# Kernel tuning notes

Measured on AMD Instinct MI355X. Metric: run time of the kernel, lower is better.

The kernel has to match this reference:

```python
import jax, jax.numpy as jnp
import numpy as np

EPS = 1e-6  # epsilon used to snap near-zero plane distances (Moller-style robustness)


def _interval(p, d):
    """Interval of the intersection line covered by a triangle.
    p: [..., 3] projections of the 3 vertices onto the intersection-line axis.
    d: [..., 3] signed distances of the 3 vertices to the other triangle's plane.
    Returns (tmin, tmax); invalid (non-straddling) -> (+inf, -inf).
    """
    nxt = jnp.array([1, 2, 0])
    di, dj = d, d[..., nxt]
    pi, pj = p, p[..., nxt]
    # edge crosses the plane iff endpoint distances have opposite signs
    # (or exactly one endpoint lies on the plane)
    valid = (di * dj <= 0) & ~((di == 0) & (dj == 0))
    denom = di - dj
    t = pi + (pj - pi) * di / jnp.where(denom == 0, 1.0, denom)
    tmin = jnp.min(jnp.where(valid, t, jnp.inf), axis=-1)
    tmax = jnp.max(jnp.where(valid, t, -jnp.inf), axis=-1)
    return tmin, tmax


def _pairwise_intersect(T):
    """Moller-style triangle-triangle intersection test for all N^2 pairs.
    T: [N, 3, 3] triangle soup. Returns bool [N, N].
    """
    N = T.shape[0]
    n = jnp.cross(T[:, 1] - T[:, 0], T[:, 2] - T[:, 0])   # [N,3] plane normals
    d = -jnp.sum(n * T[:, 0], axis=-1)                      # [N] plane offsets
    # signed distances: verts of triangle b to plane of triangle u (dv), and vice versa (du)
    dv = jnp.einsum('bvc,nc->bnv', T, n) + d[None, :, None]  # [N,N,3]
    du = jnp.einsum('nvc,bc->bnv', T, n) + d[:, None, None]  # [N,N,3]
    dv = jnp.where(jnp.abs(dv) < EPS, 0.0, dv)
    du = jnp.where(jnp.abs(du) < EPS, 0.0, du)
    # all vertices strictly on one side -> no intersection
    ssv = jnp.all(dv > 0, -1) | jnp.all(dv < 0, -1)
    ssu = jnp.all(du > 0, -1) | jnp.all(du < 0, -1)
    # direction of plane-plane intersection line; project onto its dominant axis
    D = jnp.cross(n[:, None, :], n[None, :, :])              # [N,N,3]
    ax = jnp.argmax(jnp.abs(D), axis=-1)                     # [N,N]
    idx = jnp.broadcast_to(ax[..., None, None], (N, N, 3, 1))
    pv = jnp.take_along_axis(jnp.broadcast_to(T[:, None], (N, N, 3, 3)), idx, -1)[..., 0]
    pu = jnp.take_along_axis(jnp.broadcast_to(T[None, :], (N, N, 3, 3)), idx, -1)[..., 0]
    t0v, t1v = _interval(pv, dv)
    t0u, t1u = _interval(pu, du)
    overlap = jnp.maximum(t0v, t0u) <= jnp.minimum(t1v, t1u)
    return ~ssv & ~ssu & overlap


def setup_inputs() -> dict:
    key = jax.random.key(0)
    triangles = jax.random.normal(key, (2048, 3, 3), dtype=jnp.float32)
    return {"triangles": triangles}


def reference(triangles):
    # CPU extension produces the strictly-upper-triangular pairwise matrix;
    # the torch wrapper symmetrizes it and adds the identity.
    N = triangles.shape[0]
    M = _pairwise_intersect(triangles).astype(jnp.float32)
    S = jnp.triu(M, 1)
    return S + S.T + jnp.eye(N, dtype=jnp.float32)
```

## Files before the change

### kernel.cpp

```cpp
#include <hip/hip_runtime.h>
#include <math.h>


static constexpr float EPS_SNAP = 1e-6f;
static constexpr int TS = 32;

__device__ __forceinline__ float snapz(float x) {
    return (fabsf(x) < EPS_SNAP) ? 0.0f : x;
}

__device__ __forceinline__ void tri_interval(const float p[3], const float d[3],
                                             float& tmin, float& tmax) {
#pragma clang fp contract(off)
    tmin = INFINITY;
    tmax = -INFINITY;
#pragma unroll
    for (int e = 0; e < 3; ++e) {
        const int i0 = e;
        const int i1 = (e + 1) % 3;
        const float di = d[i0], dj = d[i1];
        const float pi = p[i0], pj = p[i1];
        const bool valid = (di * dj <= 0.0f) && !((di == 0.0f) && (dj == 0.0f));
        const float denom = di - dj;
        const float dsafe = (denom == 0.0f) ? 1.0f : denom;
        const float t = pi + ((pj - pi) * di) / dsafe;
        if (valid) {
            tmin = fminf(tmin, t);
            tmax = fmaxf(tmax, t);
        }
    }
}

__global__ __launch_bounds__(256) void plane_kernel(
    const float* __restrict__ tri, float4* __restrict__ planes, int n)
{
#pragma clang fp contract(off)
    const int i = blockIdx.x * 256 + threadIdx.x;
    if (i >= n) return;
    const float* A = tri + (size_t)i * 9;
    float Av[9];
#pragma unroll
    for (int k = 0; k < 9; ++k) Av[k] = A[k];
    const float e1x = Av[3] - Av[0], e1y = Av[4] - Av[1], e1z = Av[5] - Av[2];
    const float e2x = Av[6] - Av[0], e2y = Av[7] - Av[1], e2z = Av[8] - Av[2];
    const float nx = e1y * e2z - e1z * e2y;
    const float ny = e1z * e2x - e1x * e2z;
    const float nz = e1x * e2y - e1y * e2x;
    const float d = -(((nx * Av[0]) + (ny * Av[1])) + (nz * Av[2]));
    planes[i] = make_float4(nx, ny, nz, d);
}

__global__ __launch_bounds__(1024) void tile_kernel(
    const float* __restrict__ tri, const float4* __restrict__ planes,
    float* __restrict__ out, int n)
{
#pragma clang fp contract(off)
    const int tc = blockIdx.x, tr = blockIdx.y;
    if (tr > tc) return;
    const int C = tc * TS, R = tr * TS;

    __shared__ float As[TS][13];
    __shared__ float Sres[TS][TS + 1];

    const int tx = threadIdx.x;
    const int ty = threadIdx.y;

    if (ty == 0) {
        const float* a = tri + (size_t)(R + tx) * 9;
#pragma unroll
        for (int k = 0; k < 9; ++k) As[tx][k] = a[k];
        const float4 p = planes[R + tx];
        As[tx][9] = p.x; As[tx][10] = p.y; As[tx][11] = p.z; As[tx][12] = p.w;
    }

    const int j = C + tx;
    const float* b = tri + (size_t)j * 9;
    float Bv[9];
#pragma unroll
    for (int k = 0; k < 9; ++k) Bv[k] = b[k];
    const float4 pb = planes[j];
    const float nbx = pb.x, nby = pb.y, nbz = pb.z, db = pb.w;

    __syncthreads();

    const int i = R + ty;
    float Av[9];
#pragma unroll
    for (int k = 0; k < 9; ++k) Av[k] = As[ty][k];
    const float nax = As[ty][9], nay = As[ty][10], naz = As[ty][11], da = As[ty][12];

    float dv[3], du[3];
#pragma unroll
    for (int v = 0; v < 3; ++v) {
        dv[v] = snapz((((Av[3 * v] * nbx) + (Av[3 * v + 1] * nby)) + (Av[3 * v + 2] * nbz)) + db);
        du[v] = snapz((((Bv[3 * v] * nax) + (Bv[3 * v + 1] * nay)) + (Bv[3 * v + 2] * naz)) + da);
    }

    const bool ssv = (dv[0] > 0.0f && dv[1] > 0.0f && dv[2] > 0.0f) ||
                     (dv[0] < 0.0f && dv[1] < 0.0f && dv[2] < 0.0f);
    const bool ssu = (du[0] > 0.0f && du[1] > 0.0f && du[2] > 0.0f) ||
                     (du[0] < 0.0f && du[1] < 0.0f && du[2] < 0.0f);

    const float Dx = nay * nbz - naz * nby;
    const float Dy = naz * nbx - nax * nbz;
    const float Dz = nax * nby - nay * nbx;
    const float m0 = fabsf(Dx), m1 = fabsf(Dy), m2 = fabsf(Dz);
    int axm = 0;
    float mm = m0;
    if (m1 > mm) { axm = 1; mm = m1; }
    if (m2 > mm) { axm = 2; }

    float pv[3], pu[3];
#pragma unroll
    for (int v = 0; v < 3; ++v) {
        pv[v] = (axm == 0) ? Av[3 * v] : ((axm == 1) ? Av[3 * v + 1] : Av[3 * v + 2]);
        pu[v] = (axm == 0) ? Bv[3 * v] : ((axm == 1) ? Bv[3 * v + 1] : Bv[3 * v + 2]);
    }

    float t0v, t1v, t0u, t1u;
    tri_interval(pv, dv, t0v, t1v);
    tri_interval(pu, du, t0u, t1u);

    const bool overlap = fmaxf(t0v, t0u) <= fminf(t1v, t1u);
    const bool hit = (!ssv) && (!ssu) && overlap;

    float res = hit ? 1.0f : 0.0f;
    if (i == j) res = 1.0f;

    out[(size_t)i * n + j] = res;

    if (tr != tc) {
        Sres[ty][tx] = res;
        __syncthreads();
        out[(size_t)(C + ty) * n + (R + tx)] = Sres[tx][ty];
    }
}

extern "C" void kernel_launch(void* const* d_in, const int* in_sizes, int n_in,
                              void* d_out, int out_size, void* d_ws, size_t ws_size,
                              hipStream_t stream) {
    const float* tri = (const float*)d_in[0];
    float* out = (float*)d_out;
    const int n = in_sizes[0] / 9;
    float4* planes = (float4*)d_ws;

    plane_kernel<<<(n + 255) / 256, 256, 0, stream>>>(tri, planes, n);

    dim3 block(TS, TS);
    dim3 grid(n / TS, n / TS);
    tile_kernel<<<grid, block, 0, stream>>>(tri, planes, out, n);
}
```

Measured before the change: 80.22 us.

## Use 64x64 upper-triangular tiles with linear grid and shared staging of both triangle sets

Tiles grow to 64x64, and each 64x8 block loops over eight rows per thread. The launch now covers only upper-triangular tiles through a linearized 1D grid, instead of launching the full square grid and exiting early. Both row and column triangles and their planes are staged cooperatively into shared memory with float4 loads. This cuts wasted block launches and redundant global loads, at the cost of a serial loop that decodes each tile index and of more shared memory per block.

Result: no change. 79.52 us (-0.9%).

```diff
diff --git a/kernel.cpp b/kernel.cpp
--- a/kernel.cpp
+++ b/kernel.cpp
@@ -3,7 +3,7 @@
 
 
 static constexpr float EPS_SNAP = 1e-6f;
-static constexpr int TS = 32;
+static constexpr int TS = 64;
 
 __device__ __forceinline__ float snapz(float x) {
     return (fabsf(x) < EPS_SNAP) ? 0.0f : x;
@@ -50,89 +50,104 @@
     planes[i] = make_float4(nx, ny, nz, d);
 }
 
-__global__ __launch_bounds__(1024) void tile_kernel(
+__global__ __launch_bounds__(512, 4) void tile_kernel(
     const float* __restrict__ tri, const float4* __restrict__ planes,
     float* __restrict__ out, int n)
 {
 #pragma clang fp contract(off)
-    const int tc = blockIdx.x, tr = blockIdx.y;
-    if (tr > tc) return;
-    const int C = tc * TS, R = tr * TS;
+    const int nt = n / TS;
+    int k = blockIdx.x, tr = 0;
+    while (k >= nt - tr) { k -= nt - tr; ++tr; }
+    const int tc = tr + k;
+    const int R = tr * TS, C = tc * TS;
 
-    __shared__ float As[TS][13];
-    __shared__ float Sres[TS][TS + 1];
+    __shared__ float  Asf[TS * 9];
+    __shared__ float  Bsf[TS * 9];
+    __shared__ float4 Ap[TS], Bp[TS];
+    __shared__ float  Sres[TS][TS + 1];
 
     const int tx = threadIdx.x;
     const int ty = threadIdx.y;
+    const int t = ty * TS + tx;
 
-    if (ty == 0) {
-        const float* a = tri + (size_t)(R + tx) * 9;
+    if (t < 144) {
+        ((float4*)Asf)[t] = ((const float4*)(tri + (size_t)R * 9))[t];
+    } else if (t < 288) {
+        ((float4*)Bsf)[t - 144] = ((const float4*)(tri + (size_t)C * 9))[t - 144];
+    } else if (t < 352) {
+        Ap[t - 288] = planes[R + (t - 288)];
+    } else if (t < 416) {
+        Bp[t - 352] = planes[C + (t - 352)];
+    }
+    __syncthreads();
+
+    const int j = C + tx;
+    float Bv[9];
 #pragma unroll
-        for (int k = 0; k < 9; ++k) As[tx][k] = a[k];
-        const float4 p = planes[R + tx];
-        As[tx][9] = p.x; As[tx][10] = p.y; As[tx][11] = p.z; As[tx][12] = p.w;
+    for (int kk = 0; kk < 9; ++kk) Bv[kk] = Bsf[tx * 9 + kk];
+    const float4 pb = Bp[tx];
+    const float nbx = pb.x, nby = pb.y, nbz = pb.z, db = pb.w;
+
+#pragma unroll 2
+    for (int kk = 0; kk < 8; ++kk) {
+        const int r = ty + 8 * kk;
+        const int i = R + r;
+
+        float Av[9];
+#pragma unroll
+        for (int q = 0; q < 9; ++q) Av[q] = Asf[r * 9 + q];
+        const float4 pa = Ap[r];
+        const float nax = pa.x, nay = pa.y, naz = pa.z, da = pa.w;
+
+        float dv[3], du[3];
+#pragma unroll
+        for (int v = 0; v < 3; ++v) {
+            dv[v] = snapz((((Av[3 * v] * nbx) + (Av[3 * v + 1] * nby)) + (Av[3 * v + 2] * nbz)) + db);
+            du[v] = snapz((((Bv[3 * v] * nax) + (Bv[3 * v + 1] * nay)) + (Bv[3 * v + 2] * naz)) + da);
+        }
+
+        const bool ssv = (dv[0] > 0.0f && dv[1] > 0.0f && dv[2] > 0.0f) ||
+                         (dv[0] < 0.0f && dv[1] < 0.0f && dv[2] < 0.0f);
+        const bool ssu = (du[0] > 0.0f && du[1] > 0.0f && du[2] > 0.0f) ||
+                         (du[0] < 0.0f && du[1] < 0.0f && du[2] < 0.0f);
+
+        const float Dx = nay * nbz - naz * nby;
+        const float Dy = naz * nbx - nax * nbz;
+        const float Dz = nax * nby - nay * nbx;
+        const float m0 = fabsf(Dx), m1 = fabsf(Dy), m2 = fabsf(Dz);
+        int axm = 0;
+        float mm = m0;
+        if (m1 > mm) { axm = 1; mm = m1; }
+        if (m2 > mm) { axm = 2; }
+
+        float pv[3], pu[3];
+#pragma unroll
+        for (int v = 0; v < 3; ++v) {
+            pv[v] = (axm == 0) ? Av[3 * v] : ((axm == 1) ? Av[3 * v + 1] : Av[3 * v + 2]);
+            pu[v] = (axm == 0) ? Bv[3 * v] : ((axm == 1) ? Bv[3 * v + 1] : Bv[3 * v + 2]);
+        }
+
+        float t0v, t1v, t0u, t1u;
+        tri_interval(pv, dv, t0v, t1v);
+        tri_interval(pu, du, t0u, t1u);
+
+        const bool overlap = fmaxf(t0v, t0u) <= fminf(t1v, t1u);
+        const bool hit = (!ssv) && (!ssu) && overlap;
+
+        float res = hit ? 1.0f : 0.0f;
+        if (i == j) res = 1.0f;
+
+        out[(size_t)i * n + j] = res;
+        Sres[r][tx] = res;
     }
 
-    const int j = C + tx;
-    const float* b = tri + (size_t)j * 9;
-    float Bv[9];
-#pragma unroll
-    for (int k = 0; k < 9; ++k) Bv[k] = b[k];
-    const float4 pb = planes[j];
-    const float nbx = pb.x, nby = pb.y, nbz = pb.z, db = pb.w;
-
-    __syncthreads();
-
-    const int i = R + ty;
-    float Av[9];
-#pragma unroll
-    for (int k = 0; k < 9; ++k) Av[k] = As[ty][k];
-    const float nax = As[ty][9], nay = As[ty][10], naz = As[ty][11], da = As[ty][12];
-
-    float dv[3], du[3];
-#pragma unroll
-    for (int v = 0; v < 3; ++v) {
-        dv[v] = snapz((((Av[3 * v] * nbx) + (Av[3 * v + 1] * nby)) + (Av[3 * v + 2] * nbz)) + db);
-        du[v] = snapz((((Bv[3 * v] * nax) + (Bv[3 * v + 1] * nay)) + (Bv[3 * v + 2] * naz)) + da);
-    }
-
-    const bool ssv = (dv[0] > 0.0f && dv[1] > 0.0f && dv[2] > 0.0f) ||
-                     (dv[0] < 0.0f && dv[1] < 0.0f && dv[2] < 0.0f);
-    const bool ssu = (du[0] > 0.0f && du[1] > 0.0f && du[2] > 0.0f) ||
-                     (du[0] < 0.0f && du[1] < 0.0f && du[2] < 0.0f);
-
-    const float Dx = nay * nbz - naz * nby;
-    const float Dy = naz * nbx - nax * nbz;
-    const float Dz = nax * nby - nay * nbx;
-    const float m0 = fabsf(Dx), m1 = fabsf(Dy), m2 = fabsf(Dz);
-    int axm = 0;
-    float mm = m0;
-    if (m1 > mm) { axm = 1; mm = m1; }
-    if (m2 > mm) { axm = 2; }
-
-    float pv[3], pu[3];
-#pragma unroll
-    for (int v = 0; v < 3; ++v) {
-        pv[v] = (axm == 0) ? Av[3 * v] : ((axm == 1) ? Av[3 * v + 1] : Av[3 * v + 2]);
-        pu[v] = (axm == 0) ? Bv[3 * v] : ((axm == 1) ? Bv[3 * v + 1] : Bv[3 * v + 2]);
-    }
-
-    float t0v, t1v, t0u, t1u;
-    tri_interval(pv, dv, t0v, t1v);
-    tri_interval(pu, du, t0u, t1u);
-
-    const bool overlap = fmaxf(t0v, t0u) <= fminf(t1v, t1u);
-    const bool hit = (!ssv) && (!ssu) && overlap;
-
-    float res = hit ? 1.0f : 0.0f;
-    if (i == j) res = 1.0f;
-
-    out[(size_t)i * n + j] = res;
-
     if (tr != tc) {
-        Sres[ty][tx] = res;
         __syncthreads();
-        out[(size_t)(C + ty) * n + (R + tx)] = Sres[tx][ty];
+#pragma unroll 2
+        for (int kk = 0; kk < 8; ++kk) {
+            const int c = ty + 8 * kk;
+            out[(size_t)(C + c) * n + (R + tx)] = Sres[tx][c];
+        }
     }
 }
 
@@ -146,7 +161,8 @@
 
     plane_kernel<<<(n + 255) / 256, 256, 0, stream>>>(tri, planes, n);
 
-    dim3 block(TS, TS);
-    dim3 grid(n / TS, n / TS);
-    tile_kernel<<<grid, block, 0, stream>>>(tri, planes, out, n);
+    const int nt = n / TS;
+    const int nblocks = nt * (nt + 1) / 2;
+    dim3 block(TS, 8);
+    tile_kernel<<<nblocks, block, 0, stream>>>(tri, planes, out, n);
 }
```

## Replace shared-memory tiled kernel with per-pair threads and direct symmetric stores

Applied to the files above, without the earlier changes.

Replaces the 32x32 tile kernel, which staged row triangles and the transposed result in shared memory, with 64x4 blocks where each thread loads its row triangle via a wave-uniform scalar index and writes both the (i,j) and (j,i) outputs directly. This removes shared memory staging and block-wide barriers and allows higher occupancy. In exchange, the transposed store becomes strided across lanes (uncoalesced), and many blocks in the lower triangle launch only to exit.

New measurement: 83.90 us. +4.6%, slower.

```diff
diff --git a/kernel.cpp b/kernel.cpp
--- a/kernel.cpp
+++ b/kernel.cpp
@@ -3,7 +3,6 @@
 
 
 static constexpr float EPS_SNAP = 1e-6f;
-static constexpr int TS = 32;
 
 __device__ __forceinline__ float snapz(float x) {
     return (fabsf(x) < EPS_SNAP) ? 0.0f : x;
@@ -50,44 +49,30 @@
     planes[i] = make_float4(nx, ny, nz, d);
 }
 
-__global__ __launch_bounds__(1024) void tile_kernel(
+__global__ __launch_bounds__(256, 4) void pair_kernel(
     const float* __restrict__ tri, const float4* __restrict__ planes,
     float* __restrict__ out, int n)
 {
 #pragma clang fp contract(off)
-    const int tc = blockIdx.x, tr = blockIdx.y;
-    if (tr > tc) return;
-    const int C = tc * TS, R = tr * TS;
+    const int j = blockIdx.x * 64 + threadIdx.x;
+    const int i = blockIdx.y * 4 + threadIdx.y;
+    if (i > j) return;
+    if (i == j) { out[(size_t)i * n + j] = 1.0f; return; }
 
-    __shared__ float As[TS][13];
-    __shared__ float Sres[TS][TS + 1];
+    const int iu = __builtin_amdgcn_readfirstlane(i);
+    const float* __restrict__ A = tri + (size_t)iu * 9;
+    float Av[9];
+#pragma unroll
+    for (int k = 0; k < 9; ++k) Av[k] = A[k];
+    const float4 pa = planes[iu];
+    const float nax = pa.x, nay = pa.y, naz = pa.z, da = pa.w;
 
-    const int tx = threadIdx.x;
-    const int ty = threadIdx.y;
-
-    if (ty == 0) {
-        const float* a = tri + (size_t)(R + tx) * 9;
-#pragma unroll
-        for (int k = 0; k < 9; ++k) As[tx][k] = a[k];
-        const float4 p = planes[R + tx];
-        As[tx][9] = p.x; As[tx][10] = p.y; As[tx][11] = p.z; As[tx][12] = p.w;
-    }
-
-    const int j = C + tx;
-    const float* b = tri + (size_t)j * 9;
+    const float* __restrict__ B = tri + (size_t)j * 9;
     float Bv[9];
 #pragma unroll
-    for (int k = 0; k < 9; ++k) Bv[k] = b[k];
+    for (int k = 0; k < 9; ++k) Bv[k] = B[k];
     const float4 pb = planes[j];
     const float nbx = pb.x, nby = pb.y, nbz = pb.z, db = pb.w;
-
-    __syncthreads();
-
-    const int i = R + ty;
-    float Av[9];
-#pragma unroll
-    for (int k = 0; k < 9; ++k) Av[k] = As[ty][k];
-    const float nax = As[ty][9], nay = As[ty][10], naz = As[ty][11], da = As[ty][12];
 
     float dv[3], du[3];
 #pragma unroll
@@ -123,17 +108,10 @@
 
     const bool overlap = fmaxf(t0v, t0u) <= fminf(t1v, t1u);
     const bool hit = (!ssv) && (!ssu) && overlap;
-
-    float res = hit ? 1.0f : 0.0f;
-    if (i == j) res = 1.0f;
+    const float res = hit ? 1.0f : 0.0f;
 
     out[(size_t)i * n + j] = res;
-
-    if (tr != tc) {
-        Sres[ty][tx] = res;
-        __syncthreads();
-        out[(size_t)(C + ty) * n + (R + tx)] = Sres[tx][ty];
-    }
+    out[(size_t)j * n + i] = res;
 }
 
 extern "C" void kernel_launch(void* const* d_in, const int* in_sizes, int n_in,
@@ -146,7 +124,7 @@
 
     plane_kernel<<<(n + 255) / 256, 256, 0, stream>>>(tri, planes, n);
 
-    dim3 block(TS, TS);
-    dim3 grid(n / TS, n / TS);
-    tile_kernel<<<grid, block, 0, stream>>>(tri, planes, out, n);
+    dim3 block(64, 4);
+    dim3 grid((n + 63) / 64, (n + 3) / 4);
+    pair_kernel<<<grid, block, 0, stream>>>(tri, planes, out, n);
 }
```
